# Kernel optimization log

Hardware: AMD Instinct MI355X
Metric: run time of the kernel (lower is better)

Reference implementation:

```python
import jax, jax.numpy as jnp
import numpy as np

B, H, W, C = 32, 256, 256, 4
KH, KW, F = 5, 5, 8


def setup_inputs() -> dict:
    key = jax.random.key(0)
    kx, kk = jax.random.split(key)
    x = jax.random.normal(kx, (B, H, W, C), dtype=jnp.float32)
    kernel = jax.random.normal(kk, (KH, KW, C, F), dtype=jnp.float32) * 0.1
    return {"x": x, "kernel": kernel}


def reference(x, kernel):
    """Multi-filter grayscale erosion (min-plus correlation), channels-last.

    out[b, y, x, f] = min_{dy, dx, c} ( x[b, y+dy, x+dx, c] - kernel[dy, dx, c, f] )
    (stride 1, VALID padding, rates 1 -- matching tf.nn.erosion2d followed by
    a min-reduction over the input-channel axis, per output filter.)
    """
    kh, kw, c, f = kernel.shape
    b, h, w, _ = x.shape
    ho, wo = h - kh + 1, w - kw + 1  # VALID output size
    out = None
    # Fixed, small structural loop over the kh*kw window taps; each tap is a
    # fully vectorized shifted slice + min-plus reduction over channels.
    for i in range(kh):
        for j in range(kw):
            patch = x[:, i:i + ho, j:j + wo, :]                      # [B,Ho,Wo,C]
            # min over channels of (patch - kernel tap): [B,Ho,Wo,F]
            v = jnp.min(patch[..., :, None] - kernel[i, j][None, None, None, :, :], axis=3)
            out = v if out is None else jnp.minimum(out, v)
    return out
```

## Files before the change

kernel.cpp:

```cpp
#include <hip/hip_runtime.h>

#define BB 32
#define HH 256
#define WW 256
#define CC 4
#define KH 5
#define KW 5
#define FF 8
#define HO (HH - KH + 1)
#define WO (WW - KW + 1)

__global__ __launch_bounds__(256) void erosion2d_kernel(
    const float* __restrict__ x,
    const float* __restrict__ k,
    float* __restrict__ out)
{
    const int total = BB * HO * WO;
    int tid = blockIdx.x * blockDim.x + threadIdx.x;
    if (tid >= total) return;

    int b   = tid / (HO * WO);
    int rem = tid - b * (HO * WO);
    int y   = rem / WO;
    int xo  = rem - y * WO;

    const float* xb = x + (((size_t)b * HH + y) * WW + xo) * CC;

    float acc[FF];
#pragma unroll
    for (int f = 0; f < FF; ++f) acc[f] = 3.0e38f;

#pragma unroll
    for (int dy = 0; dy < KH; ++dy) {
#pragma unroll
        for (int dx = 0; dx < KW; ++dx) {
            const float4 px = *reinterpret_cast<const float4*>(xb + (dy * WW + dx) * CC);
            const float* kp = k + ((dy * KW + dx) * CC) * FF;
#pragma unroll
            for (int f = 0; f < FF; ++f) {
                float d0 = px.x - kp[0 * FF + f];
                float d1 = px.y - kp[1 * FF + f];
                float d2 = px.z - kp[2 * FF + f];
                float d3 = px.w - kp[3 * FF + f];
                acc[f] = fminf(fminf(acc[f], fminf(d0, d1)), fminf(d2, d3));
            }
        }
    }

    float* op = out + (size_t)tid * FF;
    float4 o0 = make_float4(acc[0], acc[1], acc[2], acc[3]);
    float4 o1 = make_float4(acc[4], acc[5], acc[6], acc[7]);
    *reinterpret_cast<float4*>(op)     = o0;
    *reinterpret_cast<float4*>(op + 4) = o1;
}

extern "C" void kernel_launch(void* const* d_in, const int* in_sizes, int n_in,
                              void* d_out, int out_size, void* d_ws, size_t ws_size,
                              hipStream_t stream) {
    const float* x = (const float*)d_in[0];
    const float* k = (const float*)d_in[1];
    float* out = (float*)d_out;

    const int total = BB * HO * WO;
    const int block = 256;
    const int grid  = (total + block - 1) / block;

    erosion2d_kernel<<<grid, block, 0, stream>>>(x, k, out);
}
```

Before: 65.62 us.

## Compute erosion in packed fp16 with two output pixels per thread

Converts inputs and kernel taps to packed half2 and performs the subtract/min in packed fp16 arithmetic. Each thread now produces two adjacent output pixels, reusing loaded input columns across both. A small pre-kernel packs the filter weights into a workspace buffer. The aim is to cut ALU instruction count and redundant loads, at the cost of fp16 precision (round-toward-zero conversion), which may exceed the accuracy tolerance, plus an extra kernel launch.

```diff
diff --git a/kernel.cpp b/kernel.cpp
--- a/kernel.cpp
+++ b/kernel.cpp
@@ -9,49 +9,87 @@
 #define FF 8
 #define HO (HH - KH + 1)
 #define WO (WW - KW + 1)
+#define PX 2
+#define WOP (WO / PX)
 
-__global__ __launch_bounds__(256) void erosion2d_kernel(
+typedef _Float16 h2     __attribute__((ext_vector_type(2)));
+typedef __fp16   fp16x2 __attribute__((ext_vector_type(2)));
+
+static __device__ __forceinline__ h2 pkrtz(float a, float b) {
+    fp16x2 r = __builtin_amdgcn_cvt_pkrtz(a, b);
+    return __builtin_bit_cast(h2, r);
+}
+
+__global__ void pack_kernel(const float* __restrict__ k, unsigned int* __restrict__ kp)
+{
+    int i = blockIdx.x * blockDim.x + threadIdx.x;
+    if (i >= KH * KW * FF * 2) return;
+    int t = i >> 4;
+    int r = i & 15;
+    int f = r >> 1;
+    int p = r & 1;
+    float a = k[(t * CC + 2 * p + 0) * FF + f];
+    float b = k[(t * CC + 2 * p + 1) * FF + f];
+    kp[i] = __builtin_bit_cast(unsigned int, pkrtz(a, b));
+}
+
+__global__ __launch_bounds__(256) void erosion2d_f16(
     const float* __restrict__ x,
-    const float* __restrict__ k,
+    const h2* __restrict__ k2,
     float* __restrict__ out)
 {
-    const int total = BB * HO * WO;
+    const int total = BB * HO * WOP;
     int tid = blockIdx.x * blockDim.x + threadIdx.x;
     if (tid >= total) return;
 
-    int b   = tid / (HO * WO);
-    int rem = tid - b * (HO * WO);
-    int y   = rem / WO;
-    int xo  = rem - y * WO;
+    int b   = tid / (HO * WOP);
+    int rem = tid - b * (HO * WOP);
+    int y   = rem / WOP;
+    int xo  = (rem - y * WOP) * PX;
 
     const float* xb = x + (((size_t)b * HH + y) * WW + xo) * CC;
 
-    float acc[FF];
+    h2 acc[PX][FF];
+    const h2 big = { (_Float16)65504.0f, (_Float16)65504.0f };
 #pragma unroll
-    for (int f = 0; f < FF; ++f) acc[f] = 3.0e38f;
+    for (int p = 0; p < PX; ++p)
+#pragma unroll
+        for (int f = 0; f < FF; ++f)
+            acc[p][f] = big;
 
 #pragma unroll
     for (int dy = 0; dy < KH; ++dy) {
 #pragma unroll
-        for (int dx = 0; dx < KW; ++dx) {
-            const float4 px = *reinterpret_cast<const float4*>(xb + (dy * WW + dx) * CC);
-            const float* kp = k + ((dy * KW + dx) * CC) * FF;
+        for (int dxx = 0; dxx < KW + PX - 1; ++dxx) {
+            const float4 px = *reinterpret_cast<const float4*>(xb + (dy * WW + dxx) * CC);
+            const h2 p01 = pkrtz(px.x, px.y);
+            const h2 p23 = pkrtz(px.z, px.w);
 #pragma unroll
-            for (int f = 0; f < FF; ++f) {
-                float d0 = px.x - kp[0 * FF + f];
-                float d1 = px.y - kp[1 * FF + f];
-                float d2 = px.z - kp[2 * FF + f];
-                float d3 = px.w - kp[3 * FF + f];
-                acc[f] = fminf(fminf(acc[f], fminf(d0, d1)), fminf(d2, d3));
+            for (int p = 0; p < PX; ++p) {
+                const int dx = dxx - p;
+                if (dx < 0 || dx >= KW) continue;
+                const h2* kt = k2 + ((dy * KW + dx) * FF) * 2;
+#pragma unroll
+                for (int f = 0; f < FF; ++f) {
+                    h2 d01 = p01 - kt[f * 2 + 0];
+                    h2 d23 = p23 - kt[f * 2 + 1];
+                    acc[p][f] = __builtin_elementwise_min(
+                        acc[p][f], __builtin_elementwise_min(d01, d23));
+                }
             }
         }
     }
 
-    float* op = out + (size_t)tid * FF;
-    float4 o0 = make_float4(acc[0], acc[1], acc[2], acc[3]);
-    float4 o1 = make_float4(acc[4], acc[5], acc[6], acc[7]);
-    *reinterpret_cast<float4*>(op)     = o0;
-    *reinterpret_cast<float4*>(op + 4) = o1;
+#pragma unroll
+    for (int p = 0; p < PX; ++p) {
+        float r[FF];
+#pragma unroll
+        for (int f = 0; f < FF; ++f)
+            r[f] = fminf((float)acc[p][f][0], (float)acc[p][f][1]);
+        float* op = out + ((size_t)tid * PX + p) * FF;
+        *reinterpret_cast<float4*>(op)     = make_float4(r[0], r[1], r[2], r[3]);
+        *reinterpret_cast<float4*>(op + 4) = make_float4(r[4], r[5], r[6], r[7]);
+    }
 }
 
 extern "C" void kernel_launch(void* const* d_in, const int* in_sizes, int n_in,
@@ -61,9 +99,10 @@
     const float* k = (const float*)d_in[1];
     float* out = (float*)d_out;
 
-    const int total = BB * HO * WO;
+    pack_kernel<<<2, 256, 0, stream>>>(k, (unsigned int*)d_ws);
+
+    const int total = BB * HO * WOP;
     const int block = 256;
     const int grid  = (total + block - 1) / block;
-
-    erosion2d_kernel<<<grid, block, 0, stream>>>(x, k, out);
+    erosion2d_f16<<<grid, block, 0, stream>>>(x, (const h2*)d_ws, out);
 }
```

Result: no change. 64.53 us (-1.7%).
